# Kernel optimization log

Measured on AMD Instinct MI355X. Metric: run time of the kernel, lower is better.

## Reference

```python
import jax, jax.numpy as jnp
import numpy as np

DIM_IN = 768
DIM_EMB = 512
DIM_ATTN = 384
N_EXPERTS = 13
TOP_K = 5
NUM_CLS = 2
K_INST = 100000  # instances per bag (WSI patches)


def setup_inputs() -> dict:
    key = jax.random.key(0)
    ks = jax.random.split(key, 10)
    s = 0.02  # weight init scale
    return {
        "X_tfl": jax.random.normal(ks[0], (1, N_EXPERTS, DIM_EMB), jnp.float32),
        "X": jax.random.normal(ks[1], (1, K_INST, DIM_IN), jnp.float32),
        # feat_proj: Linear(dim_in, dim_emb) + ReLU (end_with_fc=False, eval -> no dropout)
        "W_proj": (jax.random.normal(ks[2], (DIM_IN, DIM_EMB), jnp.float32) * s),
        "b_proj": jnp.zeros((DIM_EMB,), jnp.float32),
        # Attn_Net: Linear(L,D) -> Tanh -> Linear(D,1)
        "W_attn1": (jax.random.normal(ks[3], (DIM_EMB, DIM_ATTN), jnp.float32) * s),
        "b_attn1": jnp.zeros((DIM_ATTN,), jnp.float32),
        "W_attn2": (jax.random.normal(ks[4], (DIM_ATTN, 1), jnp.float32) * s),
        "b_attn2": jnp.zeros((1,), jnp.float32),
        # router: Linear(dim_emb, n_experts, bias=False)
        "W_router": (jax.random.normal(ks[5], (DIM_EMB, N_EXPERTS), jnp.float32) * s),
        # pred_head: Linear(dim_emb, num_cls)
        "W_pred": (jax.random.normal(ks[6], (DIM_EMB, NUM_CLS), jnp.float32) * s),
        "b_pred": jnp.zeros((NUM_CLS,), jnp.float32),
    }


def reference(X_tfl, X, W_proj, b_proj, W_attn1, b_attn1, W_attn2, b_attn2,
              W_router, W_pred, b_pred):
    # feat_proj (eval mode: dropout is identity)
    H = jax.nn.relu(jnp.einsum('bkc,cd->bkd', X, W_proj) + b_proj)  # [1,K,512]
    # attention pooling (Attn_Net): tanh MLP -> scalar score per instance
    scores = jnp.einsum('bkd,de->bke', jnp.tanh(H @ W_attn1 + b_attn1), W_attn2) + b_attn2  # [1,K,1]
    A = jax.nn.softmax(scores[..., 0], axis=-1)      # [1,K]
    M = jnp.einsum('bk,bkd->bd', A, H)               # [1,512] slide representation
    # router + top-k gating
    router_logits = M @ W_router                     # [1,13]
    probs = jax.nn.softmax(router_logits, axis=-1)
    weights, sel_idx = jax.lax.top_k(probs, TOP_K)   # [1,5], [1,5]
    # Identity experts: expert i output is X_tfl[0, i, :]; gather selected, weighted combine
    sel = X_tfl[0][sel_idx[0]]                       # [5,512]
    moe_output = jnp.sum(weights[0][:, None] * sel, axis=0)[None, :]  # [1,512]
    logit = moe_output @ W_pred + b_pred             # [1,2]
    return logit
```

## Files before the change

kernel.cpp:

```cpp
#include <hip/hip_runtime.h>
#include <hip/hip_bf16.h>

typedef __attribute__((ext_vector_type(8))) short short8_t;
typedef __attribute__((ext_vector_type(4))) float f32x4;
typedef __attribute__((ext_vector_type(4))) unsigned int u32x4;

#define KINST 100000
#define KPAD  100096
#define DIMIN 768
#define DIMEMB 512
#define DIMATTN 384

__device__ __forceinline__ unsigned short f2bf(float f) {
    unsigned int u = __builtin_bit_cast(unsigned int, f);
    u = u + 0x7FFFu + ((u >> 16) & 1u);
    return (unsigned short)(u >> 16);
}
__device__ __forceinline__ unsigned int packbf(float a, float b) {
    return (unsigned int)f2bf(a) | ((unsigned int)f2bf(b) << 16);
}
__device__ __forceinline__ float bf2f(unsigned short h) {
    unsigned int u = ((unsigned int)h) << 16;
    return __builtin_bit_cast(float, u);
}
__device__ __forceinline__ float fast_tanh(float x) {
    const float e2 = __expf(2.f * x);
    return (e2 - 1.f) * __builtin_amdgcn_rcpf(e2 + 1.f);
}
__device__ __forceinline__ void gll16(const unsigned short* g, unsigned short* l) {
    __builtin_amdgcn_global_load_lds(
        (const __attribute__((address_space(1))) unsigned int*)g,
        (__attribute__((address_space(3))) unsigned int*)l, 16, 0, 0);
}

__global__ __launch_bounds__(256) void k_prep(
    const float* __restrict__ Wproj, const float* __restrict__ W1,
    unsigned short* __restrict__ WpTt, unsigned short* __restrict__ W1Tt)
{
    const int idx = blockIdx.x * 256 + threadIdx.x;
    if (idx < 49152) {
        const int t = idx >> 11, r = idx & 2047;
        const int n = r >> 2, c = r & 3;
        short8_t v;
        #pragma unroll
        for (int e = 0; e < 8; ++e)
            v[e] = (short)f2bf(Wproj[(size_t)(t * 32 + c * 8 + e) * DIMEMB + n]);
        *(short8_t*)&WpTt[t * 16384 + n * 32 + c * 8] = v;
    } else {
        const int j = idx - 49152;
        const int t = j / 3072, r = j % 3072;
        const int n = r >> 3, c = r & 7;
        short8_t v;
        #pragma unroll
        for (int e = 0; e < 8; ++e)
            v[e] = (short)f2bf(W1[(size_t)(t * 64 + c * 8 + e) * DIMATTN + n]);
        *(short8_t*)&W1Tt[t * 24576 + n * 64 + c * 8] = v;
    }
}

__global__ __launch_bounds__(256, 4) void k_gemm1(
    const float* __restrict__ X,
    const unsigned short* __restrict__ WpTt,
    const float* __restrict__ bproj,
    unsigned short* __restrict__ H)
{
    __shared__ unsigned short As[2][2048];
    const int tid = threadIdx.x;
    const int lane = tid & 63, w = tid >> 6;
    const int g = lane >> 4, fr = lane & 15;
    const int bcol = blockIdx.x * 256;
    const int brow = blockIdx.y * 64;

    const int arow = tid >> 2, aq4 = tid & 3;
    int agr = brow + arow; if (agr >= KINST) agr = KINST - 1;
    const float* xsrc = X + (size_t)agr * DIMIN + aq4 * 8;
    const int awoff = arow * 32 + ((aq4 ^ ((arow >> 1) & 3)) << 3);
    const int aro = (g ^ ((fr >> 1) & 3)) << 3;

    const unsigned short* gB = WpTt + (size_t)(bcol + w * 64 + fr) * 32 + g * 8;

    f32x4 acc[4][4] = {};
    float4 xva, xvb;

    {
        float4 xa = *(const float4*)(xsrc);
        float4 xb = *(const float4*)(xsrc + 4);
        xva = *(const float4*)(xsrc + 32);
        xvb = *(const float4*)(xsrc + 36);
        u32x4 p;
        p[0] = packbf(xa.x, xa.y); p[1] = packbf(xa.z, xa.w);
        p[2] = packbf(xb.x, xb.y); p[3] = packbf(xb.z, xb.w);
        *(u32x4*)&As[0][awoff] = p;
    }
    asm volatile("s_waitcnt lgkmcnt(0)" ::: "memory");
    __builtin_amdgcn_sched_barrier(0);
    __builtin_amdgcn_s_barrier();
    __builtin_amdgcn_sched_barrier(0);

#define G1STEP(P, T)                                                           \
    {                                                                          \
                        \
        const unsigned short* gBt = gB + (size_t)(T) * 16384;                  \
        short8_t Bf[4];                                                        \
        _Pragma("unroll")                                                      \
        for (int j = 0; j < 4; ++j)                                            \
            Bf[j] = *(const short8_t*)(gBt + j * 512);                         \
                                                       \
        short8_t af[4];                                                        \
        _Pragma("unroll")                                                      \
        for (int i = 0; i < 4; ++i)                                            \
            af[i] = *(const short8_t*)&As[P][(i * 16 + fr) * 32 + aro];        \
        if ((T) < 23) {               \
            u32x4 p;                                                           \
            p[0] = packbf(xva.x, xva.y); p[1] = packbf(xva.z, xva.w);          \
            p[2] = packbf(xvb.x, xvb.y); p[3] = packbf(xvb.z, xvb.w);          \
            *(u32x4*)&As[(P) ^ 1][awoff] = p;                                  \
        }                                                                      \
        if ((T) < 22) {                   \
            xva = *(const float4*)(xsrc + ((T) + 2) * 32);                     \
            xvb = *(const float4*)(xsrc + ((T) + 2) * 32 + 4);                 \
        }                                                                      \
        if ((T) < 23) {                                                        \
            asm volatile("s_waitcnt lgkmcnt(0)" ::: "memory");                 \
            __builtin_amdgcn_sched_barrier(0);                                 \
            __builtin_amdgcn_s_barrier();                                      \
            __builtin_amdgcn_sched_barrier(0);                                 \
        }                                                                      \
        __builtin_amdgcn_s_setprio(1);                                        \
        _Pragma("unroll")                                                      \
        for (int j = 0; j < 4; ++j)                                            \
            _Pragma("unroll")                                                  \
            for (int i = 0; i < 4; ++i)                                        \
                acc[i][j] = __builtin_amdgcn_mfma_f32_16x16x32_bf16(           \
                    af[i], Bf[j], acc[i][j], 0, 0, 0);                         \
        __builtin_amdgcn_s_setprio(0);                                        \
    }

    for (int tt = 0; tt < 24; tt += 2) {
        G1STEP(0, tt);
        G1STEP(1, tt + 1);
    }
#undef G1STEP

    #pragma unroll
    for (int j = 0; j < 4; ++j) {
        const int col = bcol + w * 64 + j * 16 + fr;
        const float bias = bproj[col];
        #pragma unroll
        for (int i = 0; i < 4; ++i) {
            const int rb = brow + i * 16 + g * 4;
            #pragma unroll
            for (int r = 0; r < 4; ++r) {
                const int row = rb + r;
                const float v = fmaxf(acc[i][j][r] + bias, 0.f);
                H[(size_t)row * DIMEMB + col] = (row < KINST) ? f2bf(v) : (unsigned short)0;
            }
        }
    }
}

__global__ __launch_bounds__(512, 2) void k_gemm2(
    const unsigned short* __restrict__ H,
    const unsigned short* __restrict__ W1Tt,
    const float* __restrict__ b1,
    const float* __restrict__ W2,
    const float* __restrict__ b2,
    float* __restrict__ Spart,
    float* __restrict__ Mpart)
{
    __shared__ unsigned short As[2][4096];
    __shared__ float sred[4][128];
    __shared__ float Elds[128];
    __shared__ float ssum[8];
    __shared__ float red[8][512];
    const int tid = threadIdx.x;
    const int lane = tid & 63, w = tid >> 6;
    const int wr = w >> 2, wc = w & 3;
    const int g = lane >> 4, fr = lane & 15;
    const int brow = blockIdx.x * 128;

    const int sr = w * 16 + (lane >> 2);
    const int c_src = (lane & 3) ^ ((sr >> 1) & 3);
    const unsigned short* gA = H + (size_t)(brow + sr) * DIMEMB + c_src * 8;
    unsigned short* ldst0 = &As[0][w * 512 + lane * 8];
    unsigned short* ldst1 = &As[1][w * 512 + lane * 8];
    const int aro = (g ^ ((fr >> 1) & 3)) << 3;

    const unsigned short* gB = W1Tt + (size_t)(wc * 96 + fr) * 64 + g * 8;

    f32x4 acc[4][6] = {};

    gll16(gA, ldst0);
    asm volatile("s_waitcnt vmcnt(0)" ::: "memory");
    __builtin_amdgcn_s_barrier();

    for (int t = 0; t < 16; ++t) {
        const int buf = t & 1;
        if (t < 15) gll16(gA + (t + 1) * 32, buf ? ldst0 : ldst1);
        short8_t Bf[6];
        const unsigned short* gBt = gB + (size_t)(t >> 1) * 24576 + (t & 1) * 32;
        #pragma unroll
        for (int j = 0; j < 6; ++j)
            Bf[j] = *(const short8_t*)(gBt + j * 1024);
        short8_t af[4];
        #pragma unroll
        for (int i = 0; i < 4; ++i)
            af[i] = *(const short8_t*)&As[buf][(wr * 64 + i * 16 + fr) * 32 + aro];
        __builtin_amdgcn_s_setprio(1);
        #pragma unroll
        for (int j = 0; j < 6; ++j)
            #pragma unroll
            for (int i = 0; i < 4; ++i)
                acc[i][j] = __builtin_amdgcn_mfma_f32_16x16x32_bf16(af[i], Bf[j], acc[i][j], 0, 0, 0);
        __builtin_amdgcn_s_setprio(0);
        if (t < 15) {
            asm volatile("s_waitcnt vmcnt(0) lgkmcnt(0)" ::: "memory");
            __builtin_amdgcn_s_barrier();
        }
    }

    float ps[4][4] = {};
    #pragma unroll
    for (int j = 0; j < 6; ++j) {
        const int col = wc * 96 + j * 16 + fr;
        const float bb = b1[col], ww = W2[col];
        #pragma unroll
        for (int i = 0; i < 4; ++i)
            #pragma unroll
            for (int r = 0; r < 4; ++r)
                ps[i][r] += fast_tanh(acc[i][j][r] + bb) * ww;
    }
    #pragma unroll
    for (int off = 1; off < 16; off <<= 1)
        #pragma unroll
        for (int i = 0; i < 4; ++i)
            #pragma unroll
            for (int r = 0; r < 4; ++r)
                ps[i][r] += __shfl_xor(ps[i][r], off, 64);
    if (fr == 0) {
        #pragma unroll
        for (int i = 0; i < 4; ++i)
            #pragma unroll
            for (int r = 0; r < 4; ++r)
                sred[wc][wr * 64 + i * 16 + g * 4 + r] = ps[i][r];
    }
    __syncthreads();
    float myE = 0.f;
    if (tid < 128) {
        const int row = brow + tid;
        const float s = sred[0][tid] + sred[1][tid] + sred[2][tid] + sred[3][tid] + b2[0];
        const float e = __expf(s);
        const float eg = (row < KINST) ? e : 0.f;
        Elds[tid] = eg;
        myE = eg;
    }
    #pragma unroll
    for (int off = 1; off < 64; off <<= 1) myE += __shfl_xor(myE, off, 64);
    if (lane == 0) ssum[w] = myE;
    __syncthreads();
    if (tid == 0) {
        float tacc = 0.f;
        #pragma unroll
        for (int i = 0; i < 8; ++i) tacc += ssum[i];
        Spart[blockIdx.x] = tacc;
    }

    float pa[8] = {};
    const int hb = lane << 3;
    #pragma unroll 4
    for (int i = 0; i < 16; ++i) {
        const int r = (w << 4) + i;
        const float e = Elds[r];
        const short8_t v = *(const short8_t*)(H + (size_t)(brow + r) * DIMEMB + hb);
        #pragma unroll
        for (int j = 0; j < 8; ++j)
            pa[j] += e * bf2f((unsigned short)v[j]);
    }
    #pragma unroll
    for (int j = 0; j < 8; ++j) red[w][hb + j] = pa[j];
    __syncthreads();
    float s2 = 0.f;
    #pragma unroll
    for (int k = 0; k < 8; ++k) s2 += red[k][tid];
    Mpart[(size_t)blockIdx.x * DIMEMB + tid] = s2;
}

__global__ __launch_bounds__(1024) void k_head(
    const float* __restrict__ Spart,
    const float* __restrict__ Mpart,
    const float* __restrict__ Wr,
    const float* __restrict__ Xtfl,
    const float* __restrict__ Wp,
    const float* __restrict__ bp,
    float* __restrict__ outp)
{
    __shared__ float Mlds[512];
    __shared__ float red2[2][512];
    __shared__ float logits[13];
    __shared__ float wsel[5];
    __shared__ int isel[5];
    __shared__ float Slds;
    __shared__ float swred[16];
    __shared__ float r0s[16], r1s[16];
    const int tid = threadIdx.x, lane = tid & 63, w = tid >> 6;
    const int half = tid >> 9, d = tid & 511;

    float s = 0.f;
    for (int i = tid; i < 782; i += 1024) s += Spart[i];
    #pragma unroll
    for (int off = 1; off < 64; off <<= 1) s += __shfl_xor(s, off, 64);
    if (lane == 0) swred[w] = s;

    float m = 0.f;
    #pragma unroll 4
    for (int b = half; b < 782; b += 2) m += Mpart[(size_t)b * 512 + d];
    red2[half][d] = m;

    __syncthreads();
    if (tid == 0) {
        float t = 0.f;
        #pragma unroll
        for (int i = 0; i < 16; ++i) t += swred[i];
        Slds = t;
    }
    __syncthreads();
    if (tid < 512) {
        Mlds[tid] = (red2[0][tid] + red2[1][tid]) / Slds;
    }
    __syncthreads();
    if (tid < 13) {
        float l = 0.f;
        for (int dd = 0; dd < 512; ++dd) l += Mlds[dd] * Wr[dd * 13 + tid];
        logits[tid] = l;
    }
    __syncthreads();
    if (tid == 0) {
        float mx = -1e30f;
        for (int i = 0; i < 13; ++i) mx = fmaxf(mx, logits[i]);
        float pe[13]; float sum = 0.f;
        for (int i = 0; i < 13; ++i) { pe[i] = __expf(logits[i] - mx); sum += pe[i]; }
        unsigned used = 0;
        for (int t = 0; t < 5; ++t) {
            int bi = 0; float bv = -1.f;
            for (int i = 0; i < 13; ++i)
                if (!((used >> i) & 1u) && pe[i] > bv) { bv = pe[i]; bi = i; }
            used |= (1u << bi);
            wsel[t] = bv / sum;
            isel[t] = bi;
        }
    }
    __syncthreads();
    float p0 = 0.f, p1 = 0.f;
    if (tid < 512) {
        float mo = 0.f;
        #pragma unroll
        for (int t = 0; t < 5; ++t) mo += wsel[t] * Xtfl[isel[t] * 512 + tid];
        p0 = mo * Wp[tid * 2 + 0];
        p1 = mo * Wp[tid * 2 + 1];
    }
    #pragma unroll
    for (int off = 1; off < 64; off <<= 1) {
        p0 += __shfl_xor(p0, off, 64);
        p1 += __shfl_xor(p1, off, 64);
    }
    if (lane == 0) { r0s[w] = p0; r1s[w] = p1; }
    __syncthreads();
    if (tid == 0) {
        float a = bp[0], b = bp[1];
        for (int i = 0; i < 16; ++i) { a += r0s[i]; b += r1s[i]; }
        outp[0] = a; outp[1] = b;
    }
}

extern "C" void kernel_launch(void* const* d_in, const int* in_sizes, int n_in,
                              void* d_out, int out_size, void* d_ws, size_t ws_size,
                              hipStream_t stream)
{
    const float* Xtfl  = (const float*)d_in[0];
    const float* X     = (const float*)d_in[1];
    const float* Wproj = (const float*)d_in[2];
    const float* bproj = (const float*)d_in[3];
    const float* W1    = (const float*)d_in[4];
    const float* b1    = (const float*)d_in[5];
    const float* W2    = (const float*)d_in[6];
    const float* b2    = (const float*)d_in[7];
    const float* Wr    = (const float*)d_in[8];
    const float* Wp    = (const float*)d_in[9];
    const float* bp    = (const float*)d_in[10];
    float* out = (float*)d_out;

    char* ws = (char*)d_ws;
    size_t off = 0;
    unsigned short* H    = (unsigned short*)(ws + off); off += (size_t)KPAD * DIMEMB * 2;
    unsigned short* WpTt = (unsigned short*)(ws + off); off += (size_t)DIMEMB * DIMIN * 2;
    unsigned short* W1Tt = (unsigned short*)(ws + off); off += (size_t)DIMATTN * DIMEMB * 2;
    float* Spart = (float*)(ws + off); off += 4096;
    float* Mpart = (float*)(ws + off); off += (size_t)782 * DIMEMB * 4;

    k_prep<<<288, 256, 0, stream>>>(Wproj, W1, WpTt, W1Tt);
    k_gemm1<<<dim3(2, 1564), 256, 0, stream>>>(X, WpTt, bproj, H);
    k_gemm2<<<782, 512, 0, stream>>>(H, W1Tt, b1, W2, b2, Spart, Mpart);
    k_head<<<1, 1024, 0, stream>>>(Spart, Mpart, Wr, Xtfl, Wp, bp, out);
}
```

Before: 382.3 us.

## Fuse projection GEMM, attention GEMM and pooling into one kernel keeping H in LDS

Merges the projection GEMM and the attention-score/pooling kernel into a single kernel. Each block computes a 64-row tile of H, keeps it in swizzled shared memory as bf16, then runs the attention GEMM and the weighted pooling from LDS. This removes the round trip of the 100k×512 H buffer through global memory. X is now loaded straight into registers and packed into MFMA fragments without an LDS stage, and the block-partial reduction is split into a small two-stage reduce. The cost is a 64 KB LDS footprint per block, which lowers occupancy, and every block re-reads the full projection weights.

```diff
diff --git a/kernel.cpp b/kernel.cpp
--- a/kernel.cpp
+++ b/kernel.cpp
@@ -6,7 +6,7 @@
 typedef __attribute__((ext_vector_type(4))) unsigned int u32x4;
 
 #define KINST 100000
-#define KPAD  100096
+#define NBLK  1563
 #define DIMIN 768
 #define DIMEMB 512
 #define DIMATTN 384
@@ -26,11 +26,6 @@
 __device__ __forceinline__ float fast_tanh(float x) {
     const float e2 = __expf(2.f * x);
     return (e2 - 1.f) * __builtin_amdgcn_rcpf(e2 + 1.f);
-}
-__device__ __forceinline__ void gll16(const unsigned short* g, unsigned short* l) {
-    __builtin_amdgcn_global_load_lds(
-        (const __attribute__((address_space(1))) unsigned int*)g,
-        (__attribute__((address_space(3))) unsigned int*)l, 16, 0, 0);
 }
 
 __global__ __launch_bounds__(256) void k_prep(
@@ -58,109 +53,10 @@
     }
 }
 
-__global__ __launch_bounds__(256, 4) void k_gemm1(
+__global__ __launch_bounds__(256, 2) void k_fused(
     const float* __restrict__ X,
     const unsigned short* __restrict__ WpTt,
     const float* __restrict__ bproj,
-    unsigned short* __restrict__ H)
-{
-    __shared__ unsigned short As[2][2048];
-    const int tid = threadIdx.x;
-    const int lane = tid & 63, w = tid >> 6;
-    const int g = lane >> 4, fr = lane & 15;
-    const int bcol = blockIdx.x * 256;
-    const int brow = blockIdx.y * 64;
-
-    const int arow = tid >> 2, aq4 = tid & 3;
-    int agr = brow + arow; if (agr >= KINST) agr = KINST - 1;
-    const float* xsrc = X + (size_t)agr * DIMIN + aq4 * 8;
-    const int awoff = arow * 32 + ((aq4 ^ ((arow >> 1) & 3)) << 3);
-    const int aro = (g ^ ((fr >> 1) & 3)) << 3;
-
-    const unsigned short* gB = WpTt + (size_t)(bcol + w * 64 + fr) * 32 + g * 8;
-
-    f32x4 acc[4][4] = {};
-    float4 xva, xvb;
-
-    {
-        float4 xa = *(const float4*)(xsrc);
-        float4 xb = *(const float4*)(xsrc + 4);
-        xva = *(const float4*)(xsrc + 32);
-        xvb = *(const float4*)(xsrc + 36);
-        u32x4 p;
-        p[0] = packbf(xa.x, xa.y); p[1] = packbf(xa.z, xa.w);
-        p[2] = packbf(xb.x, xb.y); p[3] = packbf(xb.z, xb.w);
-        *(u32x4*)&As[0][awoff] = p;
-    }
-    asm volatile("s_waitcnt lgkmcnt(0)" ::: "memory");
-    __builtin_amdgcn_sched_barrier(0);
-    __builtin_amdgcn_s_barrier();
-    __builtin_amdgcn_sched_barrier(0);
-
-#define G1STEP(P, T)                                                           \
-    {                                                                          \
-                        \
-        const unsigned short* gBt = gB + (size_t)(T) * 16384;                  \
-        short8_t Bf[4];                                                        \
-        _Pragma("unroll")                                                      \
-        for (int j = 0; j < 4; ++j)                                            \
-            Bf[j] = *(const short8_t*)(gBt + j * 512);                         \
-                                                       \
-        short8_t af[4];                                                        \
-        _Pragma("unroll")                                                      \
-        for (int i = 0; i < 4; ++i)                                            \
-            af[i] = *(const short8_t*)&As[P][(i * 16 + fr) * 32 + aro];        \
-        if ((T) < 23) {               \
-            u32x4 p;                                                           \
-            p[0] = packbf(xva.x, xva.y); p[1] = packbf(xva.z, xva.w);          \
-            p[2] = packbf(xvb.x, xvb.y); p[3] = packbf(xvb.z, xvb.w);          \
-            *(u32x4*)&As[(P) ^ 1][awoff] = p;                                  \
-        }                                                                      \
-        if ((T) < 22) {                   \
-            xva = *(const float4*)(xsrc + ((T) + 2) * 32);                     \
-            xvb = *(const float4*)(xsrc + ((T) + 2) * 32 + 4);                 \
-        }                                                                      \
-        if ((T) < 23) {                                                        \
-            asm volatile("s_waitcnt lgkmcnt(0)" ::: "memory");                 \
-            __builtin_amdgcn_sched_barrier(0);                                 \
-            __builtin_amdgcn_s_barrier();                                      \
-            __builtin_amdgcn_sched_barrier(0);                                 \
-        }                                                                      \
-        __builtin_amdgcn_s_setprio(1);                                        \
-        _Pragma("unroll")                                                      \
-        for (int j = 0; j < 4; ++j)                                            \
-            _Pragma("unroll")                                                  \
-            for (int i = 0; i < 4; ++i)                                        \
-                acc[i][j] = __builtin_amdgcn_mfma_f32_16x16x32_bf16(           \
-                    af[i], Bf[j], acc[i][j], 0, 0, 0);                         \
-        __builtin_amdgcn_s_setprio(0);                                        \
-    }
-
-    for (int tt = 0; tt < 24; tt += 2) {
-        G1STEP(0, tt);
-        G1STEP(1, tt + 1);
-    }
-#undef G1STEP
-
-    #pragma unroll
-    for (int j = 0; j < 4; ++j) {
-        const int col = bcol + w * 64 + j * 16 + fr;
-        const float bias = bproj[col];
-        #pragma unroll
-        for (int i = 0; i < 4; ++i) {
-            const int rb = brow + i * 16 + g * 4;
-            #pragma unroll
-            for (int r = 0; r < 4; ++r) {
-                const int row = rb + r;
-                const float v = fmaxf(acc[i][j][r] + bias, 0.f);
-                H[(size_t)row * DIMEMB + col] = (row < KINST) ? f2bf(v) : (unsigned short)0;
-            }
-        }
-    }
-}
-
-__global__ __launch_bounds__(512, 2) void k_gemm2(
-    const unsigned short* __restrict__ H,
     const unsigned short* __restrict__ W1Tt,
     const float* __restrict__ b1,
     const float* __restrict__ W2,
@@ -168,67 +64,124 @@
     float* __restrict__ Spart,
     float* __restrict__ Mpart)
 {
-    __shared__ unsigned short As[2][4096];
-    __shared__ float sred[4][128];
-    __shared__ float Elds[128];
-    __shared__ float ssum[8];
-    __shared__ float red[8][512];
+    __shared__ unsigned short Hs[64 * 512];
+    __shared__ float sred[4][64];
+    __shared__ float Elds[64];
+    __shared__ float redp[4][512];
     const int tid = threadIdx.x;
     const int lane = tid & 63, w = tid >> 6;
-    const int wr = w >> 2, wc = w & 3;
     const int g = lane >> 4, fr = lane & 15;
-    const int brow = blockIdx.x * 128;
-
-    const int sr = w * 16 + (lane >> 2);
-    const int c_src = (lane & 3) ^ ((sr >> 1) & 3);
-    const unsigned short* gA = H + (size_t)(brow + sr) * DIMEMB + c_src * 8;
-    unsigned short* ldst0 = &As[0][w * 512 + lane * 8];
-    unsigned short* ldst1 = &As[1][w * 512 + lane * 8];
-    const int aro = (g ^ ((fr >> 1) & 3)) << 3;
-
-    const unsigned short* gB = W1Tt + (size_t)(wc * 96 + fr) * 64 + g * 8;
-
-    f32x4 acc[4][6] = {};
-
-    gll16(gA, ldst0);
-    asm volatile("s_waitcnt vmcnt(0)" ::: "memory");
-    __builtin_amdgcn_s_barrier();
-
+    const int brow = blockIdx.x * 64;
+
+    const float* xbase[4];
+    #pragma unroll
+    for (int i = 0; i < 4; ++i) {
+        int rr = brow + i * 16 + fr; if (rr >= KINST) rr = KINST - 1;
+        xbase[i] = X + (size_t)rr * DIMIN + g * 8;
+    }
+    const unsigned short* gB1 = WpTt + (size_t)(w * 128 + fr) * 32 + g * 8;
+
+    f32x4 acc[4][8] = {};
+    float4 fX[2][4][2];
+
+    #pragma unroll
+    for (int i = 0; i < 4; ++i) {
+        fX[0][i][0] = *(const float4*)(xbase[i]);
+        fX[0][i][1] = *(const float4*)(xbase[i] + 4);
+    }
+
+#define PH1(P, T)                                                              \
+    {                                                                          \
+        if ((T) < 23) {   \
+            _Pragma("unroll")                                                  \
+            for (int i = 0; i < 4; ++i) {                                      \
+                fX[(P) ^ 1][i][0] = *(const float4*)(xbase[i] + ((T) + 1) * 32);     \
+                fX[(P) ^ 1][i][1] = *(const float4*)(xbase[i] + ((T) + 1) * 32 + 4); \
+            }                                                                  \
+        }                                                                      \
+        short8_t Bf[8];                                                        \
+        const unsigned short* gBt = gB1 + (size_t)(T) * 16384;                 \
+        _Pragma("unroll")                                                      \
+        for (int j = 0; j < 8; ++j)                                            \
+            Bf[j] = *(const short8_t*)(gBt + j * 512);                         \
+        short8_t af[4];                                                        \
+        _Pragma("unroll")                                                      \
+        for (int i = 0; i < 4; ++i) {                                          \
+            u32x4 p;                                                           \
+            p[0] = packbf(fX[P][i][0].x, fX[P][i][0].y);                       \
+            p[1] = packbf(fX[P][i][0].z, fX[P][i][0].w);                       \
+            p[2] = packbf(fX[P][i][1].x, fX[P][i][1].y);                       \
+            p[3] = packbf(fX[P][i][1].z, fX[P][i][1].w);                       \
+            af[i] = __builtin_bit_cast(short8_t, p);                           \
+        }                                                                      \
+        __builtin_amdgcn_s_setprio(1);                                        \
+        _Pragma("unroll")                                                      \
+        for (int j = 0; j < 8; ++j)                                            \
+            _Pragma("unroll")                                                  \
+            for (int i = 0; i < 4; ++i)                                        \
+                acc[i][j] = __builtin_amdgcn_mfma_f32_16x16x32_bf16(           \
+                    af[i], Bf[j], acc[i][j], 0, 0, 0);                         \
+        __builtin_amdgcn_s_setprio(0);                                        \
+        if (((T) & 3) == 3) __builtin_amdgcn_s_barrier();  \
+    }
+
+    for (int tt = 0; tt < 24; tt += 2) {
+        PH1(0, tt);
+        PH1(1, tt + 1);
+    }
+#undef PH1
+
+    #pragma unroll
+    for (int j = 0; j < 8; ++j) {
+        const int col = w * 128 + j * 16 + fr;
+        const float bias = bproj[col];
+        #pragma unroll
+        for (int i = 0; i < 4; ++i) {
+            #pragma unroll
+            for (int r = 0; r < 4; ++r) {
+                const int row = i * 16 + g * 4 + r;
+                const float v = fmaxf(acc[i][j][r] + bias, 0.f);
+                const int ch = (col >> 3) ^ (row & 7);
+                Hs[row * 512 + ch * 8 + (col & 7)] = f2bf(v);
+            }
+        }
+    }
+    __syncthreads();
+
+    f32x4 a2[4][6] = {};
+    const unsigned short* gB2 = W1Tt + (size_t)(w * 96 + fr) * 64 + g * 8;
     for (int t = 0; t < 16; ++t) {
-        const int buf = t & 1;
-        if (t < 15) gll16(gA + (t + 1) * 32, buf ? ldst0 : ldst1);
         short8_t Bf[6];
-        const unsigned short* gBt = gB + (size_t)(t >> 1) * 24576 + (t & 1) * 32;
+        const unsigned short* p = gB2 + (size_t)(t >> 1) * 24576 + (t & 1) * 32;
         #pragma unroll
         for (int j = 0; j < 6; ++j)
-            Bf[j] = *(const short8_t*)(gBt + j * 1024);
+            Bf[j] = *(const short8_t*)(p + j * 1024);
         short8_t af[4];
         #pragma unroll
+        for (int i = 0; i < 4; ++i) {
+            const int row = i * 16 + fr;
+            const int ch = (t * 4 + g) ^ (row & 7);
+            af[i] = *(const short8_t*)&Hs[row * 512 + ch * 8];
+        }
+        __builtin_amdgcn_s_setprio(1);
+        #pragma unroll
+        for (int j = 0; j < 6; ++j)
+            #pragma unroll
+            for (int i = 0; i < 4; ++i)
+                a2[i][j] = __builtin_amdgcn_mfma_f32_16x16x32_bf16(af[i], Bf[j], a2[i][j], 0, 0, 0);
+        __builtin_amdgcn_s_setprio(0);
+    }
+
+    float ps[4][4] = {};
+    #pragma unroll
+    for (int j = 0; j < 6; ++j) {
+        const int col = w * 96 + j * 16 + fr;
+        const float bb = b1[col], ww = W2[col];
+        #pragma unroll
         for (int i = 0; i < 4; ++i)
-            af[i] = *(const short8_t*)&As[buf][(wr * 64 + i * 16 + fr) * 32 + aro];
-        __builtin_amdgcn_s_setprio(1);
-        #pragma unroll
-        for (int j = 0; j < 6; ++j)
-            #pragma unroll
-            for (int i = 0; i < 4; ++i)
-                acc[i][j] = __builtin_amdgcn_mfma_f32_16x16x32_bf16(af[i], Bf[j], acc[i][j], 0, 0, 0);
-        __builtin_amdgcn_s_setprio(0);
-        if (t < 15) {
-            asm volatile("s_waitcnt vmcnt(0) lgkmcnt(0)" ::: "memory");
-            __builtin_amdgcn_s_barrier();
-        }
-    }
-
-    float ps[4][4] = {};
-    #pragma unroll
-    for (int j = 0; j < 6; ++j) {
-        const int col = wc * 96 + j * 16 + fr;
-        const float bb = b1[col], ww = W2[col];
-        #pragma unroll
-        for (int i = 0; i < 4; ++i)
             #pragma unroll
             for (int r = 0; r < 4; ++r)
-                ps[i][r] += fast_tanh(acc[i][j][r] + bb) * ww;
+                ps[i][r] += fast_tanh(a2[i][j][r] + bb) * ww;
     }
     #pragma unroll
     for (int off = 1; off < 16; off <<= 1)
@@ -242,52 +195,62 @@
         for (int i = 0; i < 4; ++i)
             #pragma unroll
             for (int r = 0; r < 4; ++r)
-                sred[wc][wr * 64 + i * 16 + g * 4 + r] = ps[i][r];
-    }
-    __syncthreads();
-    float myE = 0.f;
-    if (tid < 128) {
-        const int row = brow + tid;
-        const float s = sred[0][tid] + sred[1][tid] + sred[2][tid] + sred[3][tid] + b2[0];
-        const float e = __expf(s);
-        const float eg = (row < KINST) ? e : 0.f;
-        Elds[tid] = eg;
-        myE = eg;
-    }
-    #pragma unroll
-    for (int off = 1; off < 64; off <<= 1) myE += __shfl_xor(myE, off, 64);
-    if (lane == 0) ssum[w] = myE;
-    __syncthreads();
-    if (tid == 0) {
-        float tacc = 0.f;
-        #pragma unroll
-        for (int i = 0; i < 8; ++i) tacc += ssum[i];
-        Spart[blockIdx.x] = tacc;
-    }
+                sred[w][i * 16 + g * 4 + r] = ps[i][r];
+    }
+    __syncthreads();
+    {
+        float myE = 0.f;
+        if (tid < 64) {
+            const int grow = brow + tid;
+            const float s = sred[0][tid] + sred[1][tid] + sred[2][tid] + sred[3][tid] + b2[0];
+            const float e = (grow < KINST) ? __expf(s) : 0.f;
+            Elds[tid] = e;
+            myE = e;
+        }
+        if (w == 0) {
+            #pragma unroll
+            for (int off = 1; off < 64; off <<= 1) myE += __shfl_xor(myE, off, 64);
+            if (lane == 0) Spart[blockIdx.x] = myE;
+        }
+    }
+    __syncthreads();
 
     float pa[8] = {};
-    const int hb = lane << 3;
     #pragma unroll 4
-    for (int i = 0; i < 16; ++i) {
-        const int r = (w << 4) + i;
-        const float e = Elds[r];
-        const short8_t v = *(const short8_t*)(H + (size_t)(brow + r) * DIMEMB + hb);
-        #pragma unroll
-        for (int j = 0; j < 8; ++j)
-            pa[j] += e * bf2f((unsigned short)v[j]);
-    }
-    #pragma unroll
-    for (int j = 0; j < 8; ++j) red[w][hb + j] = pa[j];
-    __syncthreads();
-    float s2 = 0.f;
-    #pragma unroll
-    for (int k = 0; k < 8; ++k) s2 += red[k][tid];
-    Mpart[(size_t)blockIdx.x * DIMEMB + tid] = s2;
+    for (int ii = 0; ii < 16; ++ii) {
+        const int row = w * 16 + ii;
+        const float e = Elds[row];
+        const int ch = lane ^ (row & 7);
+        const short8_t v = *(const short8_t*)&Hs[row * 512 + ch * 8];
+        #pragma unroll
+        for (int jj = 0; jj < 8; ++jj)
+            pa[jj] += e * bf2f((unsigned short)v[jj]);
+    }
+    #pragma unroll
+    for (int jj = 0; jj < 8; ++jj) redp[w][lane * 8 + jj] = pa[jj];
+    __syncthreads();
+    #pragma unroll
+    for (int u = 0; u < 2; ++u) {
+        const int d = u * 256 + tid;
+        Mpart[(size_t)blockIdx.x * DIMEMB + d] =
+            redp[0][d] + redp[1][d] + redp[2][d] + redp[3][d];
+    }
+}
+
+__global__ __launch_bounds__(512) void k_red(
+    const float* __restrict__ Mpart, float* __restrict__ Mred)
+{
+    const int d = threadIdx.x;
+    const int b = blockIdx.x;
+    float m = 0.f;
+    for (int r = b; r < NBLK; r += 16)
+        m += Mpart[(size_t)r * DIMEMB + d];
+    Mred[b * DIMEMB + d] = m;
 }
 
 __global__ __launch_bounds__(1024) void k_head(
     const float* __restrict__ Spart,
-    const float* __restrict__ Mpart,
+    const float* __restrict__ Mred,
     const float* __restrict__ Wr,
     const float* __restrict__ Xtfl,
     const float* __restrict__ Wp,
@@ -295,7 +258,6 @@
     float* __restrict__ outp)
 {
     __shared__ float Mlds[512];
-    __shared__ float red2[2][512];
     __shared__ float logits[13];
     __shared__ float wsel[5];
     __shared__ int isel[5];
@@ -303,18 +265,18 @@
     __shared__ float swred[16];
     __shared__ float r0s[16], r1s[16];
     const int tid = threadIdx.x, lane = tid & 63, w = tid >> 6;
-    const int half = tid >> 9, d = tid & 511;
 
     float s = 0.f;
-    for (int i = tid; i < 782; i += 1024) s += Spart[i];
+    for (int i = tid; i < NBLK; i += 1024) s += Spart[i];
     #pragma unroll
     for (int off = 1; off < 64; off <<= 1) s += __shfl_xor(s, off, 64);
     if (lane == 0) swred[w] = s;
 
     float m = 0.f;
-    #pragma unroll 4
-    for (int b = half; b < 782; b += 2) m += Mpart[(size_t)b * 512 + d];
-    red2[half][d] = m;
+    if (tid < 512) {
+        #pragma unroll
+        for (int b = 0; b < 16; ++b) m += Mred[b * 512 + tid];
+    }
 
     __syncthreads();
     if (tid == 0) {
@@ -324,9 +286,7 @@
         Slds = t;
     }
     __syncthreads();
-    if (tid < 512) {
-        Mlds[tid] = (red2[0][tid] + red2[1][tid]) / Slds;
-    }
+    if (tid < 512) Mlds[tid] = m / Slds;
     __syncthreads();
     if (tid < 13) {
         float l = 0.f;
@@ -391,14 +351,14 @@
 
     char* ws = (char*)d_ws;
     size_t off = 0;
-    unsigned short* H    = (unsigned short*)(ws + off); off += (size_t)KPAD * DIMEMB * 2;
     unsigned short* WpTt = (unsigned short*)(ws + off); off += (size_t)DIMEMB * DIMIN * 2;
     unsigned short* W1Tt = (unsigned short*)(ws + off); off += (size_t)DIMATTN * DIMEMB * 2;
-    float* Spart = (float*)(ws + off); off += 4096;
-    float* Mpart = (float*)(ws + off); off += (size_t)782 * DIMEMB * 4;
+    float* Spart = (float*)(ws + off); off += 8192;
+    float* Mpart = (float*)(ws + off); off += (size_t)NBLK * DIMEMB * 4;
+    float* Mred  = (float*)(ws + off); off += (size_t)16 * DIMEMB * 4;
 
     k_prep<<<288, 256, 0, stream>>>(Wproj, W1, WpTt, W1Tt);
-    k_gemm1<<<dim3(2, 1564), 256, 0, stream>>>(X, WpTt, bproj, H);
-    k_gemm2<<<782, 512, 0, stream>>>(H, W1Tt, b1, W2, b2, Spart, Mpart);
-    k_head<<<1, 1024, 0, stream>>>(Spart, Mpart, Wr, Xtfl, Wp, bp, out);
-}
+    k_fused<<<NBLK, 256, 0, stream>>>(X, WpTt, bproj, W1Tt, b1, W2, b2, Spart, Mpart);
+    k_red<<<16, 512, 0, stream>>>(Mpart, Mred);
+    k_head<<<1, 1024, 0, stream>>>(Spart, Mred, Wr, Xtfl, Wp, bp, out);
+}
```

Measured after the change: 453.4 us. +18.6%, slower.
